# Performance work log

Hardware: AMD Instinct MI355X
Metric: run time of the kernel (lower is better)

Reference implementation:

```python
import jax, jax.numpy as jnp
import numpy as np

B, M_IN, H, W = 8, 63, 480, 640
VALID_FRAC = 0.05  # sparse-depth valid pixel density
N_ITERS = 5


def setup_inputs() -> dict:
    key = jax.random.key(0)
    k1, k2, k3 = jax.random.split(key, 3)
    bases = jax.random.normal(k1, (B, M_IN, H, W), dtype=jnp.float32)
    logit = jax.random.normal(k2, (B, 1, H, W), dtype=jnp.float32)
    valid = jax.random.uniform(k3, (B, 1, H, W)) < VALID_FRAC
    # invalid sparse-depth pixels -> log(0) = -inf, ignored via isfinite mask
    targets = jnp.where(valid, logit, -jnp.inf)
    return {"bases": bases, "targets": targets}


def _fit_single(basis, target):
    # basis: (m,h,w), target: (1,h,w)
    m = basis.shape[0]
    y = target[0]                                   # (h,w)
    mask = jnp.isfinite(y)
    maskf = mask.astype(basis.dtype)
    Xf = (basis * maskf).reshape(m, -1)             # masked basis, (m, hw)
    yf = jnp.where(mask, y, 0.0).reshape(-1)        # (hw,)
    XtX = Xf @ Xf.T                                 # (m,m) over valid pixels only
    Xty = Xf @ yf                                   # (m,)
    N = maskf.sum()

    # eval-mode EM-like refinement (prior.use == False): Tr_d = M / beta
    beta0 = jnp.sqrt(N)
    beta = beta0
    done = jnp.array(False)
    for _ in range(N_ITERS):
        w = jnp.linalg.solve(XtX * beta, Xty * beta)    # LU solve
        E_d = jnp.sum((yf - w @ Xf) ** 2)               # residual on valid pixels
        Tr_d = m / beta
        beta_new = N / (E_d + Tr_d)
        conv = jnp.abs(beta_new / beta0 - 1.0) < 0.02
        beta = jnp.where(done, beta, beta_new)
        beta0 = jnp.where(done, beta0, beta_new)
        done = done | conv

    A = XtX * beta
    w = jnp.linalg.solve(A, Xty * beta)                 # (m,)

    # recon3d: predicted log depth
    logit_pred = jnp.einsum('m,mhw->hw', w, basis)[None]  # (1,h,w)

    # pred_var: S_inv via Cholesky, var = (S_inv @ bt * bt).sum(0)
    L = jnp.linalg.cholesky(A)
    S_inv = jax.scipy.linalg.cho_solve((L, True), jnp.eye(m, dtype=basis.dtype))
    bt = basis.reshape(m, -1)                           # (m, hw)
    var = jnp.sum((S_inv @ bt) * bt, axis=0).reshape(1, basis.shape[1], basis.shape[2])
    return logit_pred, w, var


def reference(bases, targets):
    # th_homogenize(append=False): prepend a constant ones basis channel
    ones = jnp.ones_like(bases[:, :1])
    basis_h = jnp.concatenate([ones, bases], axis=1)    # (b, m+1, h, w)
    logits, weights, logit_var = jax.vmap(_fit_single)(basis_h, targets)
    return logits, weights, logit_var
```

## Files before the change

kernel.cpp:

```cpp
#include <hip/hip_runtime.h>
#include <cmath>

#define HW 307200
#define NB 8
#define NBASE 63
#define NSLAB (HW/64)
#define GRAM_BLKS 128

#define XTY_OFF 0
#define YTY_OFF (NB*64)
#define NC_OFF  (YTY_OFF + NB)
#define ZERO_FLOATS (NC_OFF + NB)
#define XTX_OFF ZERO_FLOATS
#define MP_OFF  (XTX_OFF + NB*64*64)
#define WV_OFF  (MP_OFF + NB*64*64)

#define OUT_W   (NB*HW)
#define OUT_VAR (OUT_W + NB*64)

__device__ __forceinline__ bool finitef(float x) {
    return (__float_as_uint(x) & 0x7f800000u) != 0x7f800000u;
}

__global__ __launch_bounds__(256, 4) void gram_kernel(
    const float* __restrict__ bases, const float* __restrict__ targets,
    float* __restrict__ ws, float* __restrict__ part)
{
    __shared__ float tile[128*68];
    __shared__ float sy[128];

    const int t  = threadIdx.x;
    const int b  = blockIdx.y;
    const int wv = t >> 6;
    const int l  = t & 63;
    const int ti = l >> 3, tj = l & 7;
    const int qq = t & 15;
    const int c  = t >> 4;

    float acc[8][8];
#pragma unroll
    for (int i = 0; i < 8; i++)
#pragma unroll
        for (int j = 0; j < 8; j++) acc[i][j] = 0.f;
    float acc_xty = 0.f, acc_yty = 0.f, acc_n = 0.f;

    const float* __restrict__ basesb = bases + (long)b * NBASE * HW;
    const float* __restrict__ targb  = targets + (long)b * HW;

    auto compute_tile = [&](int base) {
#pragma unroll 2
        for (int pp = 0; pp < 16; ++pp) {
            const int p2 = base + wv * 16 + pp;
            const float4 r0 = *(const float4*)&tile[p2*68 + 8*ti];
            const float4 r1 = *(const float4*)&tile[p2*68 + 8*ti + 4];
            const float4 c0 = *(const float4*)&tile[p2*68 + 8*tj];
            const float4 c1 = *(const float4*)&tile[p2*68 + 8*tj + 4];
            const float rr[8] = {r0.x,r0.y,r0.z,r0.w,r1.x,r1.y,r1.z,r1.w};
            const float cc[8] = {c0.x,c0.y,c0.z,c0.w,c1.x,c1.y,c1.z,c1.w};
#pragma unroll
            for (int i = 0; i < 8; i++)
#pragma unroll
                for (int j = 0; j < 8; j++)
                    acc[i][j] = fmaf(rr[i], cc[j], acc[i][j]);
            acc_xty = fmaf(sy[p2], tile[p2*68 + l], acc_xty);
        }
    };

    int fill = 0, comp = 0;

    for (int s = blockIdx.x; s < NSLAB; s += GRAM_BLKS) {
        const int pix0 = s * 64;
        const float4 ty = *(const float4*)&targb[pix0 + 4*qq];
        const bool f0 = finitef(ty.x), f1 = finitef(ty.y);
        const bool f2 = finitef(ty.z), f3 = finitef(ty.w);
        const unsigned M0 = (unsigned)__ballot(f0) & 0xFFFFu;
        const unsigned M1 = (unsigned)__ballot(f1) & 0xFFFFu;
        const unsigned M2 = (unsigned)__ballot(f2) & 0xFFFFu;
        const unsigned M3 = (unsigned)__ballot(f3) & 0xFFFFu;
        const int vc = __popc(M0) + __popc(M1) + __popc(M2) + __popc(M3);

        if (vc) {
            const unsigned lowq = (1u << qq) - 1u;
            const int pre = __popc(M0 & lowq) + __popc(M1 & lowq)
                          + __popc(M2 & lowq) + __popc(M3 & lowq);
            const int s0 = fill + pre;
            const int s1 = s0 + (int)((M0 >> qq) & 1u);
            const int s2 = s1 + (int)((M1 >> qq) & 1u);
            const int s3 = s2 + (int)((M2 >> qq) & 1u);

            if (t < 16) {
                if (f0) { acc_yty = fmaf(ty.x, ty.x, acc_yty); acc_n += 1.f; }
                if (f1) { acc_yty = fmaf(ty.y, ty.y, acc_yty); acc_n += 1.f; }
                if (f2) { acc_yty = fmaf(ty.z, ty.z, acc_yty); acc_n += 1.f; }
                if (f3) { acc_yty = fmaf(ty.w, ty.w, acc_yty); acc_n += 1.f; }
            }

            float4 v[4];
#pragma unroll
            for (int k = 0; k < 4; k++) {
                const int cb = c + 16*k;
                if (cb < 63)
                    v[k] = *(const float4*)&basesb[(long)cb * HW + pix0 + 4*qq];
            }
#pragma unroll
            for (int i = 0; i < 4; i++) {
                const bool fi = (i == 0) ? f0 : (i == 1) ? f1 : (i == 2) ? f2 : f3;
                if (fi) {
                    const int si  = (i == 0) ? s0 : (i == 1) ? s1 : (i == 2) ? s2 : s3;
                    const int row = si & 127;
#pragma unroll
                    for (int k = 0; k < 4; k++) {
                        const int cb = c + 16*k;
                        if (cb < 63) {
                            const float vi = (i == 0) ? v[k].x : (i == 1) ? v[k].y
                                           : (i == 2) ? v[k].z : v[k].w;
                            tile[row*68 + cb + 1] = vi;
                        }
                    }
                    if (c == 15) {
                        tile[row*68] = 1.f;
                        sy[row] = (i == 0) ? ty.x : (i == 1) ? ty.y
                                : (i == 2) ? ty.z : ty.w;
                    }
                }
            }
            fill += vc;
        } else {
        }

        if (fill - comp >= 64) {
            __syncthreads();
            compute_tile(comp & 127);
            comp += 64;
            __syncthreads();
        }
    }

    const int pending = fill - comp;
    if (pending > 0) {
        const int padto = comp + ((pending + 63) & ~63);
        for (int rr = fill + wv; rr < padto; rr += 4) {
            const int row = rr & 127;
            tile[row*68 + l] = 0.f;
            if (l == 0) sy[row] = 0.f;
        }
        __syncthreads();
        for (int base = comp; base < padto; base += 64) {
            compute_tile(base & 127);
            __syncthreads();
        }
    }
    __syncthreads();

    for (int w = 0; w < 4; ++w) {
        if (wv == w) {
#pragma unroll
            for (int i = 0; i < 8; i++)
#pragma unroll
                for (int j2 = 0; j2 < 8; j2++) {
                    const int e = (8*ti + i) * 64 + 8*tj + j2;
                    tile[e] = (w == 0) ? acc[i][j2] : tile[e] + acc[i][j2];
                }
        }
        __syncthreads();
    }
    float* __restrict__ pb = part + (long)(b * GRAM_BLKS + blockIdx.x) * 4096;
#pragma unroll
    for (int k = 0; k < 4; ++k)
        *(float4*)&pb[t*16 + 4*k] = *(const float4*)&tile[t*16 + 4*k];

    for (int w = 0; w < 4; ++w) {
        if (wv == w) tile[4096 + l] = (w == 0) ? acc_xty : tile[4096 + l] + acc_xty;
        __syncthreads();
    }
    if (t < 64) atomicAdd(&ws[XTY_OFF + b*64 + t], tile[4096 + t]);

#pragma unroll
    for (int off = 32; off; off >>= 1) {
        acc_yty += __shfl_down(acc_yty, off, 64);
        acc_n   += __shfl_down(acc_n,   off, 64);
    }
    if (l == 0) {
        atomicAdd(&ws[YTY_OFF + b], acc_yty);
        atomicAdd(&ws[NC_OFF  + b], acc_n);
    }
}

__global__ __launch_bounds__(256) void reduce_kernel(
    const float* __restrict__ part, float* __restrict__ ws)
{
    const int b = blockIdx.y;
    const int e = blockIdx.x * 256 + threadIdx.x;
    const float* __restrict__ pb = part + (long)b * GRAM_BLKS * 4096 + e;
    float s = 0.f;
#pragma unroll 8
    for (int k = 0; k < GRAM_BLKS; ++k)
        s += pb[(long)k * 4096];
    ws[XTX_OFF + b*4096 + e] = s;
}

__global__ __launch_bounds__(64) void solve_kernel(
    float* __restrict__ ws, float* __restrict__ out)
{
    __shared__ float A[64*65];
    __shared__ float d0[64], dinv_s[64], xty_s[64], wv_s[64];

    const int b = blockIdx.x;
    const int t = threadIdx.x;
    const float* XtX = ws + XTX_OFF + b * 4096;

    for (int e = t; e < 4096; e += 64)
        A[(e >> 6) * 65 + (e & 63)] = XtX[e];
    xty_s[t] = ws[XTY_OFF + b*64 + t];
    const float yty = ws[YTY_OFF + b];
    const float Nc  = ws[NC_OFF  + b];
    __syncthreads();
    d0[t] = A[t*65 + t];
    __syncthreads();

    for (int k = 0; k < 64; k++) {
        const float akk = A[k*65 + k];
        __syncthreads();
        const float dk = sqrtf(akk);
        if (t == k)      A[k*65 + k] = dk;
        else if (t > k)  A[t*65 + k] /= dk;
        __syncthreads();
        if (t > k) {
            const float ltk = A[t*65 + k];
            for (int j = k + 1; j <= t; j++)
                A[t*65 + j] -= ltk * A[j*65 + k];
        }
        __syncthreads();
    }

    dinv_s[t] = 1.f / A[t*65 + t];
    __syncthreads();

    float Wc[64];
#pragma unroll
    for (int i = 0; i < 64; i++) {
        float s0 = (i == t) ? 1.f : 0.f, s1 = 0.f, s2 = 0.f, s3 = 0.f;
        const int nfull = i >> 2;
#pragma unroll
        for (int qd = 0; qd < nfull; qd++) {
            const int j = qd * 4;
            s0 = fmaf(-A[i*65 + j    ], Wc[j    ], s0);
            s1 = fmaf(-A[i*65 + j + 1], Wc[j + 1], s1);
            s2 = fmaf(-A[i*65 + j + 2], Wc[j + 2], s2);
            s3 = fmaf(-A[i*65 + j + 3], Wc[j + 3], s3);
        }
#pragma unroll
        for (int j = nfull * 4; j < i; j++)
            s0 = fmaf(-A[i*65 + j], Wc[j], s0);
        Wc[i] = ((s0 + s1) + (s2 + s3)) * dinv_s[i];
    }
#pragma unroll
    for (int i = 63; i >= 0; i--) {
        float s0 = Wc[i], s1 = 0.f, s2 = 0.f, s3 = 0.f;
        const int j0 = i + 1;
        const int nfull = (64 - j0) >> 2;
#pragma unroll
        for (int qd = 0; qd < nfull; qd++) {
            const int j = j0 + qd * 4;
            s0 = fmaf(-A[(j    )*65 + i], Wc[j    ], s0);
            s1 = fmaf(-A[(j + 1)*65 + i], Wc[j + 1], s1);
            s2 = fmaf(-A[(j + 2)*65 + i], Wc[j + 2], s2);
            s3 = fmaf(-A[(j + 3)*65 + i], Wc[j + 3], s3);
        }
#pragma unroll
        for (int j = j0 + nfull * 4; j < 64; j++)
            s0 = fmaf(-A[j*65 + i], Wc[j], s0);
        Wc[i] = ((s0 + s1) + (s2 + s3)) * dinv_s[i];
    }

    float w0 = 0.f, w1 = 0.f, w2 = 0.f, w3 = 0.f;
#pragma unroll
    for (int j = 0; j < 64; j += 4) {
        w0 = fmaf(Wc[j    ], xty_s[j    ], w0);
        w1 = fmaf(Wc[j + 1], xty_s[j + 1], w1);
        w2 = fmaf(Wc[j + 2], xty_s[j + 2], w2);
        w3 = fmaf(Wc[j + 3], xty_s[j + 3], w3);
    }
    const float wt = (w0 + w1) + (w2 + w3);
    wv_s[t] = wt;
    __syncthreads();

    float qt = 0.f;
#pragma unroll
    for (int j = 0; j < 64; j++) {
        const float x = (j > t) ? A[t*65 + j] : ((j == t) ? d0[t] : A[j*65 + t]);
        qt = fmaf(x, wv_s[j], qt);
    }
    float r1 = wt * xty_s[t];
    float r2 = wt * qt;
#pragma unroll
    for (int off = 32; off; off >>= 1) {
        r1 += __shfl_down(r1, off, 64);
        r2 += __shfl_down(r2, off, 64);
    }
    r1 = __shfl(r1, 0, 64);
    r2 = __shfl(r2, 0, 64);
    const float E_d = yty - 2.f * r1 + r2;

    float beta0 = sqrtf(Nc);
    float beta  = beta0;
    bool  done  = false;
#pragma unroll
    for (int it = 0; it < 5; ++it) {
        const float Tr_d = 64.f / beta;
        const float beta_new = Nc / (E_d + Tr_d);
        const bool conv = fabsf(beta_new / beta0 - 1.f) < 0.02f;
        if (!done) { beta = beta_new; beta0 = beta_new; }
        done = done || conv;
    }
    const float ib = 1.f / beta;

    out[OUT_W + b*64 + t] = wt;
    ws[WV_OFF + b*64 + t] = wt;
    float* __restrict__ Mp = ws + MP_OFF + b * 4096;
#pragma unroll
    for (int j = 0; j < 64; j++) {
        const float v = (j > t) ? 0.f : ((j == t) ? 0.5f : 1.f) * Wc[j] * ib;
        Mp[j*64 + t] = v;
    }
}

__global__ __launch_bounds__(256, 2) void predvar_kernel(
    const float* __restrict__ bases, const float* __restrict__ ws,
    float* __restrict__ out)
{
    __shared__ float Mp_s[4096];
    __shared__ float w_s[64];

    const int b = blockIdx.y;
    const int t = threadIdx.x;
    {
        const float4* __restrict__ src = (const float4*)(ws + MP_OFF + b * 4096);
        float4* dst = (float4*)Mp_s;
        for (int e = t; e < 1024; e += 256) dst[e] = src[e];
        if (t < 64) w_s[t] = ws[WV_OFF + b*64 + t];
    }
    __syncthreads();

    const int pix = (blockIdx.x * 256 + t) * 2;
    const float* basesb = bases + (long)b * NBASE * HW + pix;

    float2 bv[64];
    bv[0] = make_float2(1.f, 1.f);
#pragma unroll
    for (int c = 1; c < 64; c++)
        bv[c] = *(const float2*)&basesb[(long)(c - 1) * HW];

    float px = w_s[0], py = w_s[0];
#pragma unroll
    for (int c = 1; c < 64; c++) {
        px = fmaf(w_s[c], bv[c].x, px);
        py = fmaf(w_s[c], bv[c].y, py);
    }

    float vx = 0.f, vy = 0.f;
#pragma unroll
    for (int i = 0; i < 64; i++) {
        float sx = 0.f, sy2 = 0.f;
#pragma unroll
        for (int qd = i >> 2; qd < 16; qd++) {
            const float4 m = *(const float4*)&Mp_s[i*64 + 4*qd];
            sx  = fmaf(m.x, bv[4*qd+0].x, sx);
            sy2 = fmaf(m.x, bv[4*qd+0].y, sy2);
            sx  = fmaf(m.y, bv[4*qd+1].x, sx);
            sy2 = fmaf(m.y, bv[4*qd+1].y, sy2);
            sx  = fmaf(m.z, bv[4*qd+2].x, sx);
            sy2 = fmaf(m.z, bv[4*qd+2].y, sy2);
            sx  = fmaf(m.w, bv[4*qd+3].x, sx);
            sy2 = fmaf(m.w, bv[4*qd+3].y, sy2);
        }
        vx = fmaf(sx,  bv[i].x, vx);
        vy = fmaf(sy2, bv[i].y, vy);
    }

    *(float2*)&out[(long)b * HW + pix] = make_float2(px, py);
    *(float2*)&out[OUT_VAR + (long)b * HW + pix] = make_float2(2.f * vx, 2.f * vy);
}

extern "C" void kernel_launch(void* const* d_in, const int* in_sizes, int n_in,
                              void* d_out, int out_size, void* d_ws, size_t ws_size,
                              hipStream_t stream)
{
    const float* bases   = (const float*)d_in[0];
    const float* targets = (const float*)d_in[1];
    float* out = (float*)d_out;
    float* ws  = (float*)d_ws;

    hipMemsetAsync(d_ws, 0, ZERO_FLOATS * sizeof(float), stream);

    gram_kernel<<<dim3(GRAM_BLKS, NB), 256, 0, stream>>>(bases, targets, ws, out);
    reduce_kernel<<<dim3(16, NB), 256, 0, stream>>>(out, ws);
    solve_kernel<<<NB, 64, 0, stream>>>(ws, out);
    predvar_kernel<<<dim3(HW / 512, NB), 256, 0, stream>>>(bases, ws, out);
}
```

Baseline: 611.7 us.

## Widen gram slabs to 256 pixels and loop predvar over four chunks

```diff
diff --git a/kernel.cpp b/kernel.cpp
--- a/kernel.cpp
+++ b/kernel.cpp
@@ -4,7 +4,7 @@
 #define HW 307200
 #define NB 8
 #define NBASE 63
-#define NSLAB (HW/64)
+#define NSLAB256 (HW/256)
 #define GRAM_BLKS 128
 
 #define XTY_OFF 0
@@ -22,7 +22,7 @@
     return (__float_as_uint(x) & 0x7f800000u) != 0x7f800000u;
 }
 
-__global__ __launch_bounds__(256, 4) void gram_kernel(
+__global__ __launch_bounds__(256, 3) void gram_kernel(
     const float* __restrict__ bases, const float* __restrict__ targets,
     float* __restrict__ ws, float* __restrict__ part)
 {
@@ -34,8 +34,9 @@
     const int wv = t >> 6;
     const int l  = t & 63;
     const int ti = l >> 3, tj = l & 7;
-    const int qq = t & 15;
-    const int c  = t >> 4;
+    const int qq = t & 63;
+    const int pg = t >> 6;
+    const int g  = qq >> 4;
 
     float acc[8][8];
 #pragma unroll
@@ -68,71 +69,84 @@
 
     int fill = 0, comp = 0;
 
-    for (int s = blockIdx.x; s < NSLAB; s += GRAM_BLKS) {
-        const int pix0 = s * 64;
+    for (int s = blockIdx.x; s < NSLAB256; s += GRAM_BLKS) {
+        const int pix0 = s * 256;
+
+        float4 v[16];
+#pragma unroll
+        for (int k = 0; k < 16; k++) {
+            const int p = pg + 4*k;
+            if (p < 63)
+                v[k] = *(const float4*)&basesb[(long)p * HW + pix0 + 4*qq];
+        }
         const float4 ty = *(const float4*)&targb[pix0 + 4*qq];
         const bool f0 = finitef(ty.x), f1 = finitef(ty.y);
         const bool f2 = finitef(ty.z), f3 = finitef(ty.w);
-        const unsigned M0 = (unsigned)__ballot(f0) & 0xFFFFu;
-        const unsigned M1 = (unsigned)__ballot(f1) & 0xFFFFu;
-        const unsigned M2 = (unsigned)__ballot(f2) & 0xFFFFu;
-        const unsigned M3 = (unsigned)__ballot(f3) & 0xFFFFu;
-        const int vc = __popc(M0) + __popc(M1) + __popc(M2) + __popc(M3);
-
-        if (vc) {
-            const unsigned lowq = (1u << qq) - 1u;
-            const int pre = __popc(M0 & lowq) + __popc(M1 & lowq)
-                          + __popc(M2 & lowq) + __popc(M3 & lowq);
-            const int s0 = fill + pre;
-            const int s1 = s0 + (int)((M0 >> qq) & 1u);
-            const int s2 = s1 + (int)((M1 >> qq) & 1u);
-            const int s3 = s2 + (int)((M2 >> qq) & 1u);
-
-            if (t < 16) {
-                if (f0) { acc_yty = fmaf(ty.x, ty.x, acc_yty); acc_n += 1.f; }
-                if (f1) { acc_yty = fmaf(ty.y, ty.y, acc_yty); acc_n += 1.f; }
-                if (f2) { acc_yty = fmaf(ty.z, ty.z, acc_yty); acc_n += 1.f; }
-                if (f3) { acc_yty = fmaf(ty.w, ty.w, acc_yty); acc_n += 1.f; }
-            }
-
-            float4 v[4];
-#pragma unroll
-            for (int k = 0; k < 4; k++) {
-                const int cb = c + 16*k;
-                if (cb < 63)
-                    v[k] = *(const float4*)&basesb[(long)cb * HW + pix0 + 4*qq];
-            }
-#pragma unroll
-            for (int i = 0; i < 4; i++) {
-                const bool fi = (i == 0) ? f0 : (i == 1) ? f1 : (i == 2) ? f2 : f3;
-                if (fi) {
-                    const int si  = (i == 0) ? s0 : (i == 1) ? s1 : (i == 2) ? s2 : s3;
-                    const int row = si & 127;
-#pragma unroll
-                    for (int k = 0; k < 4; k++) {
-                        const int cb = c + 16*k;
-                        if (cb < 63) {
-                            const float vi = (i == 0) ? v[k].x : (i == 1) ? v[k].y
-                                           : (i == 2) ? v[k].z : v[k].w;
-                            tile[row*68 + cb + 1] = vi;
+        const unsigned long long M0 = __ballot(f0), M1 = __ballot(f1);
+        const unsigned long long M2 = __ballot(f2), M3 = __ballot(f3);
+
+        int vcg[4];
+#pragma unroll
+        for (int gg = 0; gg < 4; gg++) {
+            const unsigned a0 = (unsigned)((M0 >> (16*gg)) & 0xFFFFull);
+            const unsigned a1 = (unsigned)((M1 >> (16*gg)) & 0xFFFFull);
+            const unsigned a2 = (unsigned)((M2 >> (16*gg)) & 0xFFFFull);
+            const unsigned a3 = (unsigned)((M3 >> (16*gg)) & 0xFFFFull);
+            vcg[gg] = __popc(a0) + __popc(a1) + __popc(a2) + __popc(a3);
+        }
+        const unsigned mm0 = (unsigned)((M0 >> (16*g)) & 0xFFFFull);
+        const unsigned mm1 = (unsigned)((M1 >> (16*g)) & 0xFFFFull);
+        const unsigned mm2 = (unsigned)((M2 >> (16*g)) & 0xFFFFull);
+        const unsigned mm3 = (unsigned)((M3 >> (16*g)) & 0xFFFFull);
+        const unsigned lowq = (1u << (qq & 15)) - 1u;
+        const int base_my = fill + ((g > 0) ? vcg[0] : 0)
+                                 + ((g > 1) ? vcg[1] : 0)
+                                 + ((g > 2) ? vcg[2] : 0);
+        const int c0t = __popc(mm0), c1t = __popc(mm1), c2t = __popc(mm2);
+        const int s0 = base_my + __popc(mm0 & lowq);
+        const int s1 = base_my + c0t + __popc(mm1 & lowq);
+        const int s2 = base_my + c0t + c1t + __popc(mm2 & lowq);
+        const int s3 = base_my + c0t + c1t + c2t + __popc(mm3 & lowq);
+
+        if (wv == 0) {
+            if (f0) { acc_yty = fmaf(ty.x, ty.x, acc_yty); acc_n += 1.f; }
+            if (f1) { acc_yty = fmaf(ty.y, ty.y, acc_yty); acc_n += 1.f; }
+            if (f2) { acc_yty = fmaf(ty.z, ty.z, acc_yty); acc_n += 1.f; }
+            if (f3) { acc_yty = fmaf(ty.w, ty.w, acc_yty); acc_n += 1.f; }
+        }
+
+#pragma unroll
+        for (int gg = 0; gg < 4; gg++) {
+            if (g == gg) {
+#pragma unroll
+                for (int i = 0; i < 4; i++) {
+                    const bool fi = (i==0) ? f0 : (i==1) ? f1 : (i==2) ? f2 : f3;
+                    if (fi) {
+                        const int si  = (i==0) ? s0 : (i==1) ? s1 : (i==2) ? s2 : s3;
+                        const int row = si & 127;
+#pragma unroll
+                        for (int k = 0; k < 16; k++) {
+                            const int ch = pg + 4*k;
+                            if (ch < 63) {
+                                const float vi = (i==0) ? v[k].x : (i==1) ? v[k].y
+                                               : (i==2) ? v[k].z : v[k].w;
+                                tile[row*68 + ch + 1] = vi;
+                            } else {
+                                tile[row*68] = 1.f;
+                                sy[row] = (i==0) ? ty.x : (i==1) ? ty.y
+                                        : (i==2) ? ty.z : ty.w;
+                            }
                         }
-                    }
-                    if (c == 15) {
-                        tile[row*68] = 1.f;
-                        sy[row] = (i == 0) ? ty.x : (i == 1) ? ty.y
-                                : (i == 2) ? ty.z : ty.w;
                     }
                 }
             }
-            fill += vc;
-        } else {
-        }
-
-        if (fill - comp >= 64) {
-            __syncthreads();
-            compute_tile(comp & 127);
-            comp += 64;
-            __syncthreads();
+            fill += vcg[gg];
+            if (fill - comp >= 64) {
+                __syncthreads();
+                compute_tile(comp & 127);
+                comp += 64;
+                __syncthreads();
+            }
         }
     }
 
@@ -342,44 +356,48 @@
     }
     __syncthreads();
 
-    const int pix = (blockIdx.x * 256 + t) * 2;
-    const float* basesb = bases + (long)b * NBASE * HW + pix;
-
-    float2 bv[64];
-    bv[0] = make_float2(1.f, 1.f);
-#pragma unroll
-    for (int c = 1; c < 64; c++)
-        bv[c] = *(const float2*)&basesb[(long)(c - 1) * HW];
-
-    float px = w_s[0], py = w_s[0];
-#pragma unroll
-    for (int c = 1; c < 64; c++) {
-        px = fmaf(w_s[c], bv[c].x, px);
-        py = fmaf(w_s[c], bv[c].y, py);
-    }
-
-    float vx = 0.f, vy = 0.f;
-#pragma unroll
-    for (int i = 0; i < 64; i++) {
-        float sx = 0.f, sy2 = 0.f;
-#pragma unroll
-        for (int qd = i >> 2; qd < 16; qd++) {
-            const float4 m = *(const float4*)&Mp_s[i*64 + 4*qd];
-            sx  = fmaf(m.x, bv[4*qd+0].x, sx);
-            sy2 = fmaf(m.x, bv[4*qd+0].y, sy2);
-            sx  = fmaf(m.y, bv[4*qd+1].x, sx);
-            sy2 = fmaf(m.y, bv[4*qd+1].y, sy2);
-            sx  = fmaf(m.z, bv[4*qd+2].x, sx);
-            sy2 = fmaf(m.z, bv[4*qd+2].y, sy2);
-            sx  = fmaf(m.w, bv[4*qd+3].x, sx);
-            sy2 = fmaf(m.w, bv[4*qd+3].y, sy2);
-        }
-        vx = fmaf(sx,  bv[i].x, vx);
-        vy = fmaf(sy2, bv[i].y, vy);
-    }
-
-    *(float2*)&out[(long)b * HW + pix] = make_float2(px, py);
-    *(float2*)&out[OUT_VAR + (long)b * HW + pix] = make_float2(2.f * vx, 2.f * vy);
+    const int block_base = blockIdx.x * 2048;
+
+    for (int w = 0; w < 4; ++w) {
+        const int pix = block_base + w * 512 + t * 2;
+        const float* basesb = bases + (long)b * NBASE * HW + pix;
+
+        float2 bv[64];
+        bv[0] = make_float2(1.f, 1.f);
+#pragma unroll
+        for (int c = 1; c < 64; c++)
+            bv[c] = *(const float2*)&basesb[(long)(c - 1) * HW];
+
+        float px = w_s[0], py = w_s[0];
+#pragma unroll
+        for (int c = 1; c < 64; c++) {
+            px = fmaf(w_s[c], bv[c].x, px);
+            py = fmaf(w_s[c], bv[c].y, py);
+        }
+
+        float vx = 0.f, vy = 0.f;
+#pragma unroll
+        for (int i = 0; i < 64; i++) {
+            float sx = 0.f, sy2 = 0.f;
+#pragma unroll
+            for (int qd = i >> 2; qd < 16; qd++) {
+                const float4 m = *(const float4*)&Mp_s[i*64 + 4*qd];
+                sx  = fmaf(m.x, bv[4*qd+0].x, sx);
+                sy2 = fmaf(m.x, bv[4*qd+0].y, sy2);
+                sx  = fmaf(m.y, bv[4*qd+1].x, sx);
+                sy2 = fmaf(m.y, bv[4*qd+1].y, sy2);
+                sx  = fmaf(m.z, bv[4*qd+2].x, sx);
+                sy2 = fmaf(m.z, bv[4*qd+2].y, sy2);
+                sx  = fmaf(m.w, bv[4*qd+3].x, sx);
+                sy2 = fmaf(m.w, bv[4*qd+3].y, sy2);
+            }
+            vx = fmaf(sx,  bv[i].x, vx);
+            vy = fmaf(sy2, bv[i].y, vy);
+        }
+
+        *(float2*)&out[(long)b * HW + pix] = make_float2(px, py);
+        *(float2*)&out[OUT_VAR + (long)b * HW + pix] = make_float2(2.f * vx, 2.f * vy);
+    }
 }
 
 extern "C" void kernel_launch(void* const* d_in, const int* in_sizes, int n_in,
@@ -396,5 +414,5 @@
     gram_kernel<<<dim3(GRAM_BLKS, NB), 256, 0, stream>>>(bases, targets, ws, out);
     reduce_kernel<<<dim3(16, NB), 256, 0, stream>>>(out, ws);
     solve_kernel<<<NB, 64, 0, stream>>>(ws, out);
-    predvar_kernel<<<dim3(HW / 512, NB), 256, 0, stream>>>(bases, ws, out);
-}
+    predvar_kernel<<<dim3(HW / 2048, NB), 256, 0, stream>>>(bases, ws, out);
+}
```

Result: slower. 1.884 ms (+208.0%).

## Compact valid pixels per 1024-pixel window using all threads before Gram tile compute

Applied to the files above, without the earlier changes.

```diff
diff --git a/kernel.cpp b/kernel.cpp
--- a/kernel.cpp
+++ b/kernel.cpp
@@ -4,8 +4,9 @@
 #define HW 307200
 #define NB 8
 #define NBASE 63
-#define NSLAB (HW/64)
-#define GRAM_BLKS 128
+#define WPX 1024
+#define NWIN (HW/WPX)
+#define GRAM_BLKS 100
 
 #define XTY_OFF 0
 #define YTY_OFF (NB*64)
@@ -28,14 +29,13 @@
 {
     __shared__ float tile[128*68];
     __shared__ float sy[128];
+    __shared__ int   wcs[4];
 
     const int t  = threadIdx.x;
     const int b  = blockIdx.y;
     const int wv = t >> 6;
     const int l  = t & 63;
     const int ti = l >> 3, tj = l & 7;
-    const int qq = t & 15;
-    const int c  = t >> 4;
 
     float acc[8][8];
 #pragma unroll
@@ -66,89 +66,58 @@
         }
     };
 
-    int fill = 0, comp = 0;
-
-    for (int s = blockIdx.x; s < NSLAB; s += GRAM_BLKS) {
-        const int pix0 = s * 64;
-        const float4 ty = *(const float4*)&targb[pix0 + 4*qq];
+    for (int win = blockIdx.x; win < NWIN; win += GRAM_BLKS) {
+        const int pix0 = win * WPX;
+
+        const float4 ty = *(const float4*)&targb[pix0 + 4*t];
         const bool f0 = finitef(ty.x), f1 = finitef(ty.y);
         const bool f2 = finitef(ty.z), f3 = finitef(ty.w);
-        const unsigned M0 = (unsigned)__ballot(f0) & 0xFFFFu;
-        const unsigned M1 = (unsigned)__ballot(f1) & 0xFFFFu;
-        const unsigned M2 = (unsigned)__ballot(f2) & 0xFFFFu;
-        const unsigned M3 = (unsigned)__ballot(f3) & 0xFFFFu;
-        const int vc = __popc(M0) + __popc(M1) + __popc(M2) + __popc(M3);
-
-        if (vc) {
-            const unsigned lowq = (1u << qq) - 1u;
-            const int pre = __popc(M0 & lowq) + __popc(M1 & lowq)
-                          + __popc(M2 & lowq) + __popc(M3 & lowq);
-            const int s0 = fill + pre;
-            const int s1 = s0 + (int)((M0 >> qq) & 1u);
-            const int s2 = s1 + (int)((M1 >> qq) & 1u);
-            const int s3 = s2 + (int)((M2 >> qq) & 1u);
-
-            if (t < 16) {
-                if (f0) { acc_yty = fmaf(ty.x, ty.x, acc_yty); acc_n += 1.f; }
-                if (f1) { acc_yty = fmaf(ty.y, ty.y, acc_yty); acc_n += 1.f; }
-                if (f2) { acc_yty = fmaf(ty.z, ty.z, acc_yty); acc_n += 1.f; }
-                if (f3) { acc_yty = fmaf(ty.w, ty.w, acc_yty); acc_n += 1.f; }
-            }
-
-            float4 v[4];
-#pragma unroll
-            for (int k = 0; k < 4; k++) {
-                const int cb = c + 16*k;
-                if (cb < 63)
-                    v[k] = *(const float4*)&basesb[(long)cb * HW + pix0 + 4*qq];
-            }
-#pragma unroll
-            for (int i = 0; i < 4; i++) {
-                const bool fi = (i == 0) ? f0 : (i == 1) ? f1 : (i == 2) ? f2 : f3;
-                if (fi) {
-                    const int si  = (i == 0) ? s0 : (i == 1) ? s1 : (i == 2) ? s2 : s3;
-                    const int row = si & 127;
-#pragma unroll
-                    for (int k = 0; k < 4; k++) {
-                        const int cb = c + 16*k;
-                        if (cb < 63) {
-                            const float vi = (i == 0) ? v[k].x : (i == 1) ? v[k].y
-                                           : (i == 2) ? v[k].z : v[k].w;
-                            tile[row*68 + cb + 1] = vi;
-                        }
-                    }
-                    if (c == 15) {
-                        tile[row*68] = 1.f;
-                        sy[row] = (i == 0) ? ty.x : (i == 1) ? ty.y
-                                : (i == 2) ? ty.z : ty.w;
-                    }
-                }
-            }
-            fill += vc;
-        } else {
-        }
-
-        if (fill - comp >= 64) {
-            __syncthreads();
-            compute_tile(comp & 127);
-            comp += 64;
-            __syncthreads();
-        }
-    }
-
-    const int pending = fill - comp;
-    if (pending > 0) {
-        const int padto = comp + ((pending + 63) & ~63);
-        for (int rr = fill + wv; rr < padto; rr += 4) {
-            const int row = rr & 127;
-            tile[row*68 + l] = 0.f;
-            if (l == 0) sy[row] = 0.f;
-        }
-        __syncthreads();
-        for (int base = comp; base < padto; base += 64) {
-            compute_tile(base & 127);
-            __syncthreads();
-        }
+        const unsigned long long M0 = __ballot(f0), M1 = __ballot(f1);
+        const unsigned long long M2 = __ballot(f2), M3 = __ballot(f3);
+        const int c0t = __popcll(M0), c1t = __popcll(M1), c2t = __popcll(M2);
+        const int wc  = c0t + c1t + c2t + __popcll(M3);
+        if (l == 0) wcs[wv] = wc;
+
+        if (f0) { acc_yty = fmaf(ty.x, ty.x, acc_yty); acc_n += 1.f; }
+        if (f1) { acc_yty = fmaf(ty.y, ty.y, acc_yty); acc_n += 1.f; }
+        if (f2) { acc_yty = fmaf(ty.z, ty.z, acc_yty); acc_n += 1.f; }
+        if (f3) { acc_yty = fmaf(ty.w, ty.w, acc_yty); acc_n += 1.f; }
+
+        __syncthreads();
+        int wbase = 0;
+#pragma unroll
+        for (int w = 0; w < 4; ++w) if (w < wv) wbase += wcs[w];
+        const int cnt = wcs[0] + wcs[1] + wcs[2] + wcs[3];
+
+        const unsigned long long low = (1ull << l) - 1ull;
+        const int s0 = wbase + __popcll(M0 & low);
+        const int s1 = wbase + c0t + __popcll(M1 & low);
+        const int s2 = wbase + c0t + c1t + __popcll(M2 & low);
+        const int s3 = wbase + c0t + c1t + c2t + __popcll(M3 & low);
+
+        if (f0) { tile[s0*68] = 1.f; sy[s0] = ty.x; }
+        if (f1) { tile[s1*68] = 1.f; sy[s1] = ty.y; }
+        if (f2) { tile[s2*68] = 1.f; sy[s2] = ty.z; }
+        if (f3) { tile[s3*68] = 1.f; sy[s3] = ty.w; }
+
+        const float* __restrict__ bp = basesb + pix0 + 4*t;
+#pragma unroll 4
+        for (int c = 0; c < NBASE; c++) {
+            const float4 v = *(const float4*)&bp[(long)c * HW];
+            if (f0) tile[s0*68 + c + 1] = v.x;
+            if (f1) tile[s1*68 + c + 1] = v.y;
+            if (f2) tile[s2*68 + c + 1] = v.z;
+            if (f3) tile[s3*68 + c + 1] = v.w;
+        }
+
+        const int padto = (cnt + 63) & ~63;
+        for (int rr = cnt + wv; rr < padto; rr += 4) {
+            tile[rr*68 + l] = 0.f;
+            if (l == 0) sy[rr] = 0.f;
+        }
+        __syncthreads();
+        for (int base = 0; base < padto; base += 64)
+            compute_tile(base);
     }
     __syncthreads();
 
@@ -193,7 +162,7 @@
     const int e = blockIdx.x * 256 + threadIdx.x;
     const float* __restrict__ pb = part + (long)b * GRAM_BLKS * 4096 + e;
     float s = 0.f;
-#pragma unroll 8
+#pragma unroll 4
     for (int k = 0; k < GRAM_BLKS; ++k)
         s += pb[(long)k * 4096];
     ws[XTX_OFF + b*4096 + e] = s;
```

Result: slower. 638.0 us (+4.3%).
